# Kernel optimization log

Measured on AMD Instinct MI355X. Metric: run time of the kernel, lower is better.

## Reference

```python
import jax, jax.numpy as jnp
import numpy as np

B = 1 << 20
EMB = 8
N_BREEDS, N_TEMPS = 15, 9
HIDDENS = [128, 64, 32]
IN_DIM = (EMB * 2 + 9) * 2  # 50
EPS = 1e-5


def _encode_pet(breed, size, energy, temp, age, social, weight, breed_emb, temp_emb):
    # breed/temp: [B] int -> embedding gather [B,8]; size/energy -> one-hot [B,3]
    be = breed_emb[breed]
    te = temp_emb[temp]
    size_oh = jax.nn.one_hot(size, 3, dtype=be.dtype)
    energy_oh = jax.nn.one_hot(energy, 3, dtype=be.dtype)
    nums = jnp.stack([age / 15.0, social, weight / 100.0], axis=-1)  # [B,3]
    return jnp.concatenate([be, size_oh, energy_oh, te, nums], axis=-1)  # [B,25]


def _mlp(x, Ws, bs, gammas, betas, Wout, bout):
    for W, b, g, bt in zip(Ws, bs, gammas, betas):
        x = x @ W + b
        mu = jnp.mean(x, axis=0)
        var = jnp.mean(jnp.square(x - mu), axis=0)  # biased var (torch BN training)
        x = (x - mu) * jax.lax.rsqrt(var + EPS) * g + bt
        x = jax.nn.relu(x)
    x = x @ Wout + bout
    return jax.nn.sigmoid(x).squeeze(-1)  # [B]


def setup_inputs() -> dict:
    key = jax.random.key(0)
    ks = jax.random.split(key, 32)
    inp = {
        "pet1_breed": jax.random.randint(ks[0], (B,), 0, N_BREEDS, dtype=jnp.int32),
        "pet1_size": jax.random.randint(ks[1], (B,), 0, 3, dtype=jnp.int32),
        "pet1_energy": jax.random.randint(ks[2], (B,), 0, 3, dtype=jnp.int32),
        "pet1_temp": jax.random.randint(ks[3], (B,), 0, N_TEMPS, dtype=jnp.int32),
        "pet1_age": jax.random.uniform(ks[4], (B,)) * 15.0,
        "pet1_social": jax.random.uniform(ks[5], (B,)),
        "pet1_weight": jax.random.uniform(ks[6], (B,)) * 100.0,
        "pet2_breed": jax.random.randint(ks[7], (B,), 0, N_BREEDS, dtype=jnp.int32),
        "pet2_size": jax.random.randint(ks[8], (B,), 0, 3, dtype=jnp.int32),
        "pet2_energy": jax.random.randint(ks[9], (B,), 0, 3, dtype=jnp.int32),
        "pet2_temp": jax.random.randint(ks[10], (B,), 0, N_TEMPS, dtype=jnp.int32),
        "pet2_age": jax.random.uniform(ks[11], (B,)) * 15.0,
        "pet2_social": jax.random.uniform(ks[12], (B,)),
        "pet2_weight": jax.random.uniform(ks[13], (B,)) * 100.0,
        "breed_emb": jax.random.normal(ks[14], (N_BREEDS, EMB), dtype=jnp.float32),
        "temp_emb": jax.random.normal(ks[15], (N_TEMPS, EMB), dtype=jnp.float32),
    }
    prev = IN_DIM
    ki = 16
    for i, h in enumerate(HIDDENS, start=1):
        s = 1.0 / np.sqrt(prev)
        inp[f"W{i}"] = jax.random.uniform(ks[ki], (prev, h), minval=-s, maxval=s); ki += 1
        inp[f"b{i}"] = jax.random.uniform(ks[ki], (h,), minval=-s, maxval=s); ki += 1
        inp[f"gamma{i}"] = jnp.ones((h,), jnp.float32)
        inp[f"beta{i}"] = jnp.zeros((h,), jnp.float32)
        prev = h
    s = 1.0 / np.sqrt(prev)
    inp["W4"] = jax.random.uniform(ks[ki], (prev, 1), minval=-s, maxval=s); ki += 1
    inp["b4"] = jax.random.uniform(ks[ki], (1,), minval=-s, maxval=s)
    return inp


def reference(pet1_breed, pet1_size, pet1_energy, pet1_temp, pet1_age, pet1_social, pet1_weight,
              pet2_breed, pet2_size, pet2_energy, pet2_temp, pet2_age, pet2_social, pet2_weight,
              breed_emb, temp_emb,
              W1, b1, gamma1, beta1, W2, b2, gamma2, beta2, W3, b3, gamma3, beta3, W4, b4):
    f1 = _encode_pet(pet1_breed, pet1_size, pet1_energy, pet1_temp,
                     pet1_age, pet1_social, pet1_weight, breed_emb, temp_emb)
    f2 = _encode_pet(pet2_breed, pet2_size, pet2_energy, pet2_temp,
                     pet2_age, pet2_social, pet2_weight, breed_emb, temp_emb)
    x = jnp.concatenate([f1, f2], axis=-1)  # [B,50]
    return _mlp(x, [W1, W2, W3], [b1, b2, b3], [gamma1, gamma2, gamma3],
                [beta1, beta2, beta3], W4, b4)
```

## Files before the change

### kernel.cpp

```cpp
#include <hip/hip_runtime.h>
#include <hip/hip_bf16.h>

#define BATCH (1u<<20)
static constexpr float EPSBN = 1e-5f;
static constexpr float INV_B = 1.0f / (float)BATCH;

typedef unsigned int   uint;
typedef unsigned short ushort;

#define TSTR 132
#define NTABROWS 66
#define TBSTR 136
#define OFF_TBF    36864ULL
#define OFF_W2F    55296ULL
#define OFF_W3F    71680ULL
#define OFF_STATS  75776ULL
#define OFF_PARAMS 90112ULL
#define OFF_X2     98304ULL
#define T1_NEED    (98304ULL + 134217728ULL)

struct Ptrs {
  const int *br1,*sz1,*en1,*tp1; const float *ag1,*so1,*wt1;
  const int *br2,*sz2,*en2,*tp2; const float *ag2,*so2,*wt2;
  const float *bemb,*temb;
  const float *W1,*b1,*g1,*be1;
  const float *W2,*b2,*g2,*be2;
  const float *W3,*b3,*g3,*be3;
  const float *W4,*b4;
  float* ws; float* out;
};

typedef __attribute__((ext_vector_type(8))) short bf16x8;
typedef __attribute__((ext_vector_type(4))) float f32x4;

__device__ __forceinline__ float4 ld4(const float* p) {
  return *reinterpret_cast<const float4*>(p);
}
__device__ __forceinline__ void add4(float4& a, const float4 b) {
  a.x += b.x; a.y += b.y; a.z += b.z; a.w += b.w;
}
__device__ __forceinline__ void fma4s(float4& a, const float4 b, float s) {
  a.x = fmaf(b.x, s, a.x); a.y = fmaf(b.y, s, a.y);
  a.z = fmaf(b.z, s, a.z); a.w = fmaf(b.w, s, a.w);
}

__device__ __forceinline__ ushort bfb(float f) {
  union { __hip_bfloat16 h; ushort u; } cv; cv.h = __float2bfloat16(f); return cv.u;
}
__device__ __forceinline__ uint pk2(float a, float b) {
  return ((uint)bfb(b) << 16) | (uint)bfb(a);
}
__device__ __forceinline__ bf16x8 ldfrag(const void* p) {
  union { uint4 u; bf16x8 v; } cv; cv.u = *reinterpret_cast<const uint4*>(p); return cv.v;
}
__device__ __forceinline__ bf16x8 mkfrag(uint a, uint b, uint c, uint d) {
  union { uint4 u; bf16x8 v; } cv; cv.u = make_uint4(a,b,c,d); return cv.v;
}
__device__ __forceinline__ float bflo(uint w) { return __uint_as_float(w << 16); }
__device__ __forceinline__ float bfhi(uint w) { return __uint_as_float(w & 0xffff0000u); }

struct SIdx { int r[8]; float v[6]; };
__device__ __forceinline__ SIdx load_idx(const Ptrs& P, unsigned s) {
  SIdx o;
  o.r[0] = P.br1[s];      o.r[1] = 15 + P.tp1[s];
  o.r[2] = 24 + P.br2[s]; o.r[3] = 39 + P.tp2[s];
  o.r[4] = 48 + P.sz1[s]; o.r[5] = 51 + P.en1[s];
  o.r[6] = 54 + P.sz2[s]; o.r[7] = 57 + P.en2[s];
  o.v[0] = P.ag1[s]*(1.0f/15.0f); o.v[1] = P.so1[s]; o.v[2] = P.wt1[s]*0.01f;
  o.v[3] = P.ag2[s]*(1.0f/15.0f); o.v[4] = P.so2[s]; o.v[5] = P.wt2[s]*0.01f;
  return o;
}

__device__ __forceinline__ void load_rb(const Ptrs& P, unsigned s, int rb[8], float v[6]) {
  SIdx o = load_idx(P, s);
  #pragma unroll
  for (int i = 0; i < 8; ++i) rb[i] = o.r[i]*TSTR;
  #pragma unroll
  for (int i = 0; i < 6; ++i) v[i] = o.v[i];
}

__device__ __forceinline__ void stage_tab(const float* wsT, const float* params,
                                          float* Tl, bool bn1) {
  for (int i = threadIdx.x; i < NTABROWS*TSTR; i += blockDim.x) Tl[i] = wsT[i];
  if (bn1) {
    for (int i = threadIdx.x; i < 128; i += blockDim.x) {
      Tl[66*TSTR + i] = params[i];
      Tl[67*TSTR + i] = params[128 + i];
    }
  }
  __syncthreads();
}

__device__ __forceinline__ void x2_from_lds(const float* Tl, const int rb[8], const float v[6],
                                            const float* W2, const float* b2, float4 acc[16]) {
  #pragma unroll
  for (int j4 = 0; j4 < 16; ++j4) acc[j4] = ld4(b2 + j4*4);
  #pragma unroll 1
  for (int c4 = 0; c4 < 32; ++c4) {
    const int c = c4 * 4;
    float4 x = *reinterpret_cast<const float4*>(Tl + rb[0] + c);
    add4(x, *reinterpret_cast<const float4*>(Tl + rb[1] + c));
    add4(x, *reinterpret_cast<const float4*>(Tl + rb[2] + c));
    add4(x, *reinterpret_cast<const float4*>(Tl + rb[3] + c));
    add4(x, *reinterpret_cast<const float4*>(Tl + rb[4] + c));
    add4(x, *reinterpret_cast<const float4*>(Tl + rb[5] + c));
    add4(x, *reinterpret_cast<const float4*>(Tl + rb[6] + c));
    add4(x, *reinterpret_cast<const float4*>(Tl + rb[7] + c));
    #pragma unroll
    for (int m = 0; m < 6; ++m)
      fma4s(x, *reinterpret_cast<const float4*>(Tl + (60+m)*TSTR + c), v[m]);
    const float4 sc = *reinterpret_cast<const float4*>(Tl + 66*TSTR + c);
    const float4 sh = *reinterpret_cast<const float4*>(Tl + 67*TSTR + c);
    float hv[4];
    hv[0] = fmaxf(fmaf(x.x, sc.x, sh.x), 0.0f);
    hv[1] = fmaxf(fmaf(x.y, sc.y, sh.y), 0.0f);
    hv[2] = fmaxf(fmaf(x.z, sc.z, sh.z), 0.0f);
    hv[3] = fmaxf(fmaf(x.w, sc.w, sh.w), 0.0f);
    #pragma unroll
    for (int r = 0; r < 4; ++r) {
      const float hr = hv[r];
      const float4* w = reinterpret_cast<const float4*>(W2 + (c + r)*64);
      #pragma unroll
      for (int j4 = 0; j4 < 16; ++j4) fma4s(acc[j4], w[j4], hr);
    }
  }
}

__device__ __forceinline__ void x3_from_acc2(const float4 acc2[16], const Ptrs& P,
                                             const float* sc2, const float* sh2,
                                             float4 acc3[8]) {
  #pragma unroll
  for (int j4 = 0; j4 < 8; ++j4) acc3[j4] = ld4(P.b3 + j4*4);
  #pragma unroll
  for (int k4 = 0; k4 < 16; ++k4) {
    const float4 a = acc2[k4];
    const float4 sc = ld4(sc2 + k4*4), sh = ld4(sh2 + k4*4);
    const float hr[4] = {
      fmaxf(fmaf(a.x, sc.x, sh.x), 0.0f),
      fmaxf(fmaf(a.y, sc.y, sh.y), 0.0f),
      fmaxf(fmaf(a.z, sc.z, sh.z), 0.0f),
      fmaxf(fmaf(a.w, sc.w, sh.w), 0.0f)};
    #pragma unroll
    for (int r = 0; r < 4; ++r) {
      const float4* w = reinterpret_cast<const float4*>(P.W3 + (k4*4 + r)*32);
      #pragma unroll
      for (int j4 = 0; j4 < 8; ++j4) fma4s(acc3[j4], w[j4], hr[r]);
    }
  }
}

__device__ __forceinline__ float bfly_tail32(float st[32], int lane) {
#define BSTEP(D) { const bool h = (lane & D) != 0; \
  _Pragma("unroll") \
  for (int i = 0; i < D; ++i) { \
    float mine = h ? st[i] : st[i+D]; \
    float oth  = __shfl_xor(mine, D, 64); \
    float keep = h ? st[i+D] : st[i]; \
    st[i] = keep + oth; } }
  BSTEP(16) BSTEP(8) BSTEP(4) BSTEP(2) BSTEP(1)
#undef BSTEP
  return st[0];
}

template<bool SQ>
__device__ __forceinline__ float bfly64_from(const float4 acc[16], int lane) {
  float st[32];
  const bool hi = (lane & 32) != 0;
  #pragma unroll
  for (int j4 = 0; j4 < 8; ++j4) {
#define DO1(comp, idx) { \
    float lo = acc[j4].comp, hc = acc[j4+8].comp; \
    if (SQ) { lo *= lo; hc *= hc; } \
    float mine = hi ? lo : hc; \
    float keep = hi ? hc : lo; \
    st[4*j4+idx] = keep + __shfl_xor(mine, 32, 64); }
    DO1(x,0) DO1(y,1) DO1(z,2) DO1(w,3)
#undef DO1
  }
  return bfly_tail32(st, lane);
}

template<bool SQ>
__device__ __forceinline__ float bfly32_from(const float4 acc3[8], int lane) {
  float st[32];
  const bool hi = (lane & 32) != 0;
  #pragma unroll
  for (int j4 = 0; j4 < 8; ++j4) {
#define DO1(comp, idx) { \
    float vv = acc3[j4].comp; \
    if (SQ) vv *= vv; \
    float mine = hi ? vv : 0.0f; \
    float keep = hi ? 0.0f : vv; \
    st[4*j4+idx] = keep + __shfl_xor(mine, 32, 64); }
    DO1(x,0) DO1(y,1) DO1(z,2) DO1(w,3)
#undef DO1
  }
  return bfly_tail32(st, lane);
}


__global__ __launch_bounds__(256) void k_prep(Ptrs P) {
  const int t = threadIdx.x;
  float* T = P.ws;
  {
    float* st = (float*)((char*)P.ws + OFF_STATS);
    for (int i = t; i < 224*16; i += 256) st[i] = 0.0f;
  }
  if (t < 128) {
    const int c = t;
    for (int b = 0; b < 15; ++b) {
      float a1 = P.b1[c], a2 = 0.0f;
      #pragma unroll
      for (int e = 0; e < 8; ++e) {
        a1 = fmaf(P.bemb[b*8+e], P.W1[e*128 + c], a1);
        a2 = fmaf(P.bemb[b*8+e], P.W1[(25+e)*128 + c], a2);
      }
      T[b*TSTR + c] = a1; T[(24+b)*TSTR + c] = a2;
    }
    for (int tt = 0; tt < 9; ++tt) {
      float a1 = 0.0f, a2 = 0.0f;
      #pragma unroll
      for (int e = 0; e < 8; ++e) {
        a1 = fmaf(P.temb[tt*8+e], P.W1[(14+e)*128 + c], a1);
        a2 = fmaf(P.temb[tt*8+e], P.W1[(39+e)*128 + c], a2);
      }
      T[(15+tt)*TSTR + c] = a1; T[(39+tt)*TSTR + c] = a2;
    }
    #pragma unroll
    for (int i = 0; i < 3; ++i) {
      T[(48+i)*TSTR + c] = P.W1[(8+i)*128 + c];
      T[(51+i)*TSTR + c] = P.W1[(11+i)*128 + c];
      T[(54+i)*TSTR + c] = P.W1[(33+i)*128 + c];
      T[(57+i)*TSTR + c] = P.W1[(36+i)*128 + c];
    }
    const int cr[6] = {22,23,24,47,48,49};
    #pragma unroll
    for (int m = 0; m < 6; ++m) T[(60+m)*TSTR + c] = P.W1[cr[m]*128 + c];
  }
  __syncthreads();
  __hip_bfloat16* Tb = (__hip_bfloat16*)((char*)P.ws + OFF_TBF);
  for (int idx = t; idx < 66*128; idx += 256) {
    const int r = idx >> 7, c = idx & 127;
    Tb[r*TBSTR + c] = __float2bfloat16(T[r*TSTR + c]);
  }
  __hip_bfloat16* w2f = (__hip_bfloat16*)((char*)P.ws + OFF_W2F);
  for (int slot = t; slot < 1024; slot += 256) {
    const int fid = slot >> 6, l = slot & 63;
    const int mt = fid >> 2, kk = fid & 3, q = l >> 4, m = l & 15;
    #pragma unroll
    for (int e = 0; e < 8; ++e)
      w2f[slot*8 + e] = __float2bfloat16(P.W2[(kk*32 + 8*q + e)*64 + 16*mt + m]);
  }
  __hip_bfloat16* w3f = (__hip_bfloat16*)((char*)P.ws + OFF_W3F);
  for (int slot = t; slot < 256; slot += 256) {
    const int fid = slot >> 6, l = slot & 63;
    const int mt = fid >> 1, kk = fid & 1, q = l >> 4, m = l & 15;
    #pragma unroll
    for (int e = 0; e < 8; ++e)
      w3f[slot*8 + e] = __float2bfloat16(P.W3[(kk*32 + 8*q + e)*32 + 16*mt + m]);
  }
}

__global__ __launch_bounds__(512) void k_stats1(Ptrs P) {
  __shared__ __align__(16) __hip_bfloat16 Tb[60*TBSTR];
  __shared__ float sred[256];
  {
    const uint* src = (const uint*)((const char*)P.ws + OFF_TBF);
    uint* dst = (uint*)Tb;
    for (int i = threadIdx.x; i < 60*TBSTR/2; i += 512) dst[i] = src[i];
  }
  if (threadIdx.x < 256) sred[threadIdx.x] = 0.f;
  __syncthreads();
  const int lane = threadIdx.x & 63;
  const int q = lane >> 4, m16 = lane & 15;
  const __hip_bfloat16* Tbc = (const __hip_bfloat16*)((const char*)P.ws + OFF_TBF);
  const unsigned gw = (blockIdx.x*512 + threadIdx.x) >> 6;
  const unsigned nw = (gridDim.x*512) >> 6;
  const int kk = gw & 3;
  const unsigned t0 = gw >> 2, ts = nw >> 2;
  const int c = kk*32 + 8*q;
  float sums[8], sqs[8];
  #pragma unroll
  for (int i = 0; i < 8; ++i) { sums[i] = 0.f; sqs[i] = 0.f; }
  for (unsigned tt = t0; tt < (BATCH>>4); tt += ts) {
    const unsigned s = tt*16 + m16;
    const SIdx o = load_idx(P, s);
    float x[8];
    #pragma unroll
    for (int e = 0; e < 8; ++e) x[e] = 0.f;
    #pragma unroll
    for (int g = 0; g < 8; ++g) {
      const uint4 u = *reinterpret_cast<const uint4*>(Tb + o.r[g]*TBSTR + c);
      const uint w[4] = {u.x,u.y,u.z,u.w};
      #pragma unroll
      for (int j = 0; j < 4; ++j) { x[2*j] += bflo(w[j]); x[2*j+1] += bfhi(w[j]); }
    }
    #pragma unroll
    for (int m = 0; m < 6; ++m) {
      const uint4 u = *reinterpret_cast<const uint4*>(Tbc + (60+m)*TBSTR + c);
      const uint w[4] = {u.x,u.y,u.z,u.w};
      #pragma unroll
      for (int j = 0; j < 4; ++j) {
        x[2*j]   = fmaf(bflo(w[j]), o.v[m], x[2*j]);
        x[2*j+1] = fmaf(bfhi(w[j]), o.v[m], x[2*j+1]);
      }
    }
    #pragma unroll
    for (int e = 0; e < 8; ++e) {
      sums[e] += x[e];
      sqs[e]   = fmaf(x[e], x[e], sqs[e]);
    }
  }
  #pragma unroll
  for (int d = 1; d <= 8; d <<= 1) {
    #pragma unroll
    for (int i = 0; i < 8; ++i) {
      sums[i] += __shfl_xor(sums[i], d, 64);
      sqs[i]  += __shfl_xor(sqs[i],  d, 64);
    }
  }
  if (m16 == 0) {
    #pragma unroll
    for (int e = 0; e < 8; ++e) {
      atomicAdd(&sred[c + e], sums[e]);
      atomicAdd(&sred[128 + c + e], sqs[e]);
    }
  }
  __syncthreads();
  if (threadIdx.x < 128) {
    float* stat = (float*)((char*)P.ws + OFF_STATS) + (size_t)threadIdx.x*16;
    atomicAdd(stat,     sred[threadIdx.x]);
    atomicAdd(stat + 8, sred[128+threadIdx.x]);
  }
}

__global__ void k_finalize(Ptrs P, int nch, int entry0, int pofs,
                           const float* g, const float* be) {
  const int c = threadIdx.x;
  if (c >= nch) return;
  const float* stat = (const float*)((const char*)P.ws + OFF_STATS) + (size_t)(entry0 + c)*16;
  const float mean = stat[0] * INV_B;
  const float var  = stat[8] * INV_B - mean*mean;
  const float inv  = 1.0f / sqrtf(var + EPSBN);
  const float scale = g[c] * inv;
  float* params = (float*)((char*)P.ws + OFF_PARAMS);
  params[pofs + c]       = scale;
  params[pofs + nch + c] = be[c] - mean * scale;
}

__global__ __launch_bounds__(512) void k_l2m(Ptrs P) {
  __shared__ __align__(16) float Tl[60*TSTR];
  for (int i = threadIdx.x; i < 60*TSTR; i += 512) Tl[i] = P.ws[i];
  __syncthreads();
  const float* params = (const float*)((const char*)P.ws + OFF_PARAMS);
  const float* sc1 = params, *sh1 = params + 128;
  const float* contT = P.ws;
  const int lane = threadIdx.x & 63;
  const int q = lane >> 4, m16 = lane & 15;
  const char* w2fB = (const char*)P.ws + OFF_W2F;
  char* x2B = (char*)P.ws + OFF_X2;
  const unsigned nw = (gridDim.x*512) >> 6;
  const unsigned NT = BATCH >> 4;
  unsigned it = (blockIdx.x*512 + threadIdx.x) >> 6;
  if (it >= NT) return;
  SIdx cur = load_idx(P, it*16 + m16);
  while (true) {
    const unsigned itn = it + nw;
    const bool more = itn < NT;
    SIdx nxt;
    if (more) nxt = load_idx(P, itn*16 + m16);
    const unsigned s = it*16 + m16;
    int rb[8];
    #pragma unroll
    for (int i = 0; i < 8; ++i) rb[i] = cur.r[i]*TSTR;
    f32x4 D[4];
    #pragma unroll
    for (int mt = 0; mt < 4; ++mt) {
      const float4 b = ld4(P.b2 + 16*mt + 4*q);
      D[mt][0] = b.x; D[mt][1] = b.y; D[mt][2] = b.z; D[mt][3] = b.w;
    }
    #pragma unroll
    for (int kk = 0; kk < 4; ++kk) {
      const int c = kk*32 + 8*q;
      float4 xa = ld4(Tl + rb[0] + c);
      float4 xb = ld4(Tl + rb[0] + c + 4);
      #pragma unroll
      for (int g = 1; g < 8; ++g) {
        add4(xa, ld4(Tl + rb[g] + c));
        add4(xb, ld4(Tl + rb[g] + c + 4));
      }
      #pragma unroll
      for (int m = 0; m < 6; ++m) {
        fma4s(xa, ld4(contT + (60+m)*TSTR + c), cur.v[m]);
        fma4s(xb, ld4(contT + (60+m)*TSTR + c + 4), cur.v[m]);
      }
      const float4 sca = ld4(sc1 + c), sha = ld4(sh1 + c);
      const float4 scb = ld4(sc1 + c + 4), shb = ld4(sh1 + c + 4);
      const float h0 = fmaxf(fmaf(xa.x, sca.x, sha.x), 0.f);
      const float h1 = fmaxf(fmaf(xa.y, sca.y, sha.y), 0.f);
      const float h2 = fmaxf(fmaf(xa.z, sca.z, sha.z), 0.f);
      const float h3 = fmaxf(fmaf(xa.w, sca.w, sha.w), 0.f);
      const float h4 = fmaxf(fmaf(xb.x, scb.x, shb.x), 0.f);
      const float h5 = fmaxf(fmaf(xb.y, scb.y, shb.y), 0.f);
      const float h6 = fmaxf(fmaf(xb.z, scb.z, shb.z), 0.f);
      const float h7 = fmaxf(fmaf(xb.w, scb.w, shb.w), 0.f);
      const bf16x8 bf = mkfrag(pk2(h0,h1), pk2(h2,h3), pk2(h4,h5), pk2(h6,h7));
      #pragma unroll
      for (int mt = 0; mt < 4; ++mt) {
        const bf16x8 af = ldfrag(w2fB + (size_t)((mt*4+kk)*64 + lane)*16);
        D[mt] = __builtin_amdgcn_mfma_f32_16x16x32_bf16(af, bf, D[mt], 0, 0, 0);
      }
    }
    #pragma unroll
    for (int mt = 0; mt < 4; ++mt) {
      const uint lo = pk2(D[mt][0], D[mt][1]);
      const uint hi = pk2(D[mt][2], D[mt][3]);
      *reinterpret_cast<uint2*>(x2B + (size_t)s*128 + (16*mt + 4*q)*2) = make_uint2(lo, hi);
    }
    if (!more) break;
    cur = nxt; it = itn;
  }
}

__global__ __launch_bounds__(256) void k_stats2(Ptrs P) {
  const uint* x2u = (const uint*)((const char*)P.ws + OFF_X2);
  const int pid = threadIdx.x & 31;
  const int lane = threadIdx.x & 63;
  const int w = threadIdx.x >> 6;
  float slo = 0.f, shi = 0.f, qlo = 0.f, qhi = 0.f;
  const unsigned r0 = blockIdx.x*8 + (threadIdx.x >> 5);
  const unsigned rs = gridDim.x*8;
  #pragma unroll 4
  for (unsigned r = r0; r < BATCH; r += rs) {
    const uint u = x2u[(size_t)r*32 + pid];
    const float lo = bflo(u), hi = bfhi(u);
    slo += lo; shi += hi;
    qlo = fmaf(lo, lo, qlo); qhi = fmaf(hi, hi, qhi);
  }
  slo += __shfl_xor(slo, 32, 64); shi += __shfl_xor(shi, 32, 64);
  qlo += __shfl_xor(qlo, 32, 64); qhi += __shfl_xor(qhi, 32, 64);
  __shared__ float red[512];
  if (lane < 32) {
    red[w*64 + 2*pid]       = slo; red[w*64 + 2*pid + 1]       = shi;
    red[256 + w*64 + 2*pid] = qlo; red[256 + w*64 + 2*pid + 1] = qhi;
  }
  __syncthreads();
  if (threadIdx.x < 64) {
    const int c = threadIdx.x;
    const float s  = red[c] + red[64+c] + red[128+c] + red[192+c];
    const float qq = red[256+c] + red[320+c] + red[384+c] + red[448+c];
    float* stat = (float*)((char*)P.ws + OFF_STATS) + (size_t)(128 + c)*16;
    atomicAdd(stat, s); atomicAdd(stat + 8, qq);
  }
}

__global__ __launch_bounds__(256) void k_l3m(Ptrs P) {
  const float* params = (const float*)((const char*)P.ws + OFF_PARAMS);
  const float* sc2 = params + 256, *sh2 = params + 320;
  const int lane = threadIdx.x & 63;
  const int q = lane >> 4, m16 = lane & 15;
  const char* w3fB = (const char*)P.ws + OFF_W3F;
  char* xB = (char*)P.ws + OFF_X2;
  const unsigned nw = (gridDim.x*256) >> 6;
  const unsigned NT = BATCH >> 4;
  unsigned it = (blockIdx.x*256 + threadIdx.x) >> 6;
  if (it >= NT) return;
  unsigned s = it*16 + m16;
  uint4 u0 = *reinterpret_cast<const uint4*>(xB + (size_t)s*128 + q*16);
  uint4 u1 = *reinterpret_cast<const uint4*>(xB + (size_t)s*128 + 64 + q*16);
  while (true) {
    const unsigned itn = it + nw;
    const bool more = itn < NT;
    uint4 n0, n1;
    if (more) {
      const unsigned sn = itn*16 + m16;
      n0 = *reinterpret_cast<const uint4*>(xB + (size_t)sn*128 + q*16);
      n1 = *reinterpret_cast<const uint4*>(xB + (size_t)sn*128 + 64 + q*16);
    }
    f32x4 D[2];
    #pragma unroll
    for (int mt = 0; mt < 2; ++mt) {
      const float4 b = ld4(P.b3 + 16*mt + 4*q);
      D[mt][0] = b.x; D[mt][1] = b.y; D[mt][2] = b.z; D[mt][3] = b.w;
    }
    #pragma unroll
    for (int kk = 0; kk < 2; ++kk) {
      const uint4 u = (kk == 0) ? u0 : u1;
      const int c = kk*32 + 8*q;
      const float4 scA = ld4(sc2 + c), shA = ld4(sh2 + c);
      const float4 scB = ld4(sc2 + c + 4), shB = ld4(sh2 + c + 4);
      const uint w[4] = {u.x,u.y,u.z,u.w};
      const float h0 = fmaxf(fmaf(bflo(w[0]), scA.x, shA.x), 0.f);
      const float h1 = fmaxf(fmaf(bfhi(w[0]), scA.y, shA.y), 0.f);
      const float h2 = fmaxf(fmaf(bflo(w[1]), scA.z, shA.z), 0.f);
      const float h3 = fmaxf(fmaf(bfhi(w[1]), scA.w, shA.w), 0.f);
      const float h4 = fmaxf(fmaf(bflo(w[2]), scB.x, shB.x), 0.f);
      const float h5 = fmaxf(fmaf(bfhi(w[2]), scB.y, shB.y), 0.f);
      const float h6 = fmaxf(fmaf(bflo(w[3]), scB.z, shB.z), 0.f);
      const float h7 = fmaxf(fmaf(bfhi(w[3]), scB.w, shB.w), 0.f);
      const bf16x8 bf = mkfrag(pk2(h0,h1), pk2(h2,h3), pk2(h4,h5), pk2(h6,h7));
      #pragma unroll
      for (int mt = 0; mt < 2; ++mt) {
        const bf16x8 af = ldfrag(w3fB + (size_t)((mt*2+kk)*64 + lane)*16);
        D[mt] = __builtin_amdgcn_mfma_f32_16x16x32_bf16(af, bf, D[mt], 0, 0, 0);
      }
    }
    #pragma unroll
    for (int mt = 0; mt < 2; ++mt) {
      const uint lo = pk2(D[mt][0], D[mt][1]);
      const uint hi = pk2(D[mt][2], D[mt][3]);
      *reinterpret_cast<uint2*>(xB + (size_t)s*128 + (16*mt + 4*q)*2) = make_uint2(lo, hi);
    }
    if (!more) break;
    u0 = n0; u1 = n1; it = itn; s = it*16 + m16;
  }
}

__global__ __launch_bounds__(256) void k_stats3(Ptrs P) {
  const uint* xu = (const uint*)((const char*)P.ws + OFF_X2);
  const int pid = threadIdx.x & 15;
  const int lane = threadIdx.x & 63;
  const int w = threadIdx.x >> 6;
  float slo = 0.f, shi = 0.f, qlo = 0.f, qhi = 0.f;
  const unsigned r0 = blockIdx.x*16 + (threadIdx.x >> 4);
  const unsigned rs = gridDim.x*16;
  #pragma unroll 4
  for (unsigned r = r0; r < BATCH; r += rs) {
    const uint u = xu[(size_t)r*32 + pid];
    const float lo = bflo(u), hi = bfhi(u);
    slo += lo; shi += hi;
    qlo = fmaf(lo, lo, qlo); qhi = fmaf(hi, hi, qhi);
  }
  #pragma unroll
  for (int d = 16; d <= 32; d <<= 1) {
    slo += __shfl_xor(slo, d, 64); shi += __shfl_xor(shi, d, 64);
    qlo += __shfl_xor(qlo, d, 64); qhi += __shfl_xor(qhi, d, 64);
  }
  __shared__ float red[256];
  if (lane < 16) {
    red[w*32 + 2*pid]       = slo; red[w*32 + 2*pid + 1]       = shi;
    red[128 + w*32 + 2*pid] = qlo; red[128 + w*32 + 2*pid + 1] = qhi;
  }
  __syncthreads();
  if (threadIdx.x < 32) {
    const int c = threadIdx.x;
    const float s  = red[c] + red[32+c] + red[64+c] + red[96+c];
    const float qq = red[128+c] + red[160+c] + red[192+c] + red[224+c];
    float* stat = (float*)((char*)P.ws + OFF_STATS) + (size_t)(192 + c)*16;
    atomicAdd(stat, s); atomicAdd(stat + 8, qq);
  }
}

__global__ __launch_bounds__(256) void k_l4n(Ptrs P) {
  const float* params = (const float*)((const char*)P.ws + OFF_PARAMS);
  const float* sc3 = params + 384, *sh3 = params + 416;
  const char* xB = (const char*)P.ws + OFF_X2;
  const unsigned stride = gridDim.x * 256;
  for (unsigned s = blockIdx.x*256 + threadIdx.x; s < BATCH; s += stride) {
    float z = P.b4[0];
    #pragma unroll
    for (int c16 = 0; c16 < 4; ++c16) {
      const uint4 u = *reinterpret_cast<const uint4*>(xB + (size_t)s*128 + c16*16);
      const uint w[4] = {u.x,u.y,u.z,u.w};
      #pragma unroll
      for (int j = 0; j < 4; ++j) {
        const int ch = c16*8 + 2*j;
        const float hlo = fmaxf(fmaf(bflo(w[j]), sc3[ch],   sh3[ch]),   0.f);
        const float hhi = fmaxf(fmaf(bfhi(w[j]), sc3[ch+1], sh3[ch+1]), 0.f);
        z = fmaf(hlo, P.W4[ch], z);
        z = fmaf(hhi, P.W4[ch+1], z);
      }
    }
    P.out[s] = 1.0f / (1.0f + __expf(-z));
  }
}

__global__ __launch_bounds__(256) void k_l2r(Ptrs P) {
  __shared__ __align__(16) float Tl[68*TSTR];
  __shared__ float red[512];
  const float* params = (const float*)((const char*)P.ws + OFF_PARAMS);
  stage_tab(P.ws, params, Tl, true);
  const int lane = threadIdx.x & 63;
  float4 sums[16], sqs[16];
  #pragma unroll
  for (int j4 = 0; j4 < 16; ++j4) {
    sums[j4] = make_float4(0.f,0.f,0.f,0.f);
    sqs[j4]  = make_float4(0.f,0.f,0.f,0.f);
  }
  const unsigned stride = gridDim.x * 256;
  for (unsigned s = blockIdx.x*256 + threadIdx.x; s < BATCH; s += stride) {
    int rb[8]; float v[6];
    load_rb(P, s, rb, v);
    float4 acc[16];
    x2_from_lds(Tl, rb, v, P.W2, P.b2, acc);
    #pragma unroll
    for (int j4 = 0; j4 < 16; ++j4) {
      add4(sums[j4], acc[j4]);
      sqs[j4].x = fmaf(acc[j4].x, acc[j4].x, sqs[j4].x);
      sqs[j4].y = fmaf(acc[j4].y, acc[j4].y, sqs[j4].y);
      sqs[j4].z = fmaf(acc[j4].z, acc[j4].z, sqs[j4].z);
      sqs[j4].w = fmaf(acc[j4].w, acc[j4].w, sqs[j4].w);
    }
  }
  const float psum = bfly64_from<false>(sums, lane);
  const float psq  = bfly64_from<false>(sqs,  lane);
  red[threadIdx.x] = psum; red[256 + threadIdx.x] = psq;
  __syncthreads();
  const int t = threadIdx.x;
  if (t < 64) {
    const float s0 = red[t] + red[t+64] + red[t+128] + red[t+192];
    const float q0 = red[256+t] + red[256+t+64] + red[256+t+128] + red[256+t+192];
    float* stat = (float*)((char*)P.ws + OFF_STATS) + (size_t)(128 + t)*16;
    atomicAdd(stat, s0); atomicAdd(stat + 8, q0);
  }
}

__global__ __launch_bounds__(256) void k_l3_rec(Ptrs P) {
  __shared__ __align__(16) float Tl[68*TSTR];
  __shared__ float red[512];
  const float* params = (const float*)((const char*)P.ws + OFF_PARAMS);
  stage_tab(P.ws, params, Tl, true);
  const float* sc2 = params + 256, *sh2 = params + 320;
  const int lane = threadIdx.x & 63;
  float4 sums3[8], sqs3[8];
  #pragma unroll
  for (int j4 = 0; j4 < 8; ++j4) {
    sums3[j4] = make_float4(0.f,0.f,0.f,0.f);
    sqs3[j4]  = make_float4(0.f,0.f,0.f,0.f);
  }
  const unsigned stride = gridDim.x * 256;
  for (unsigned s = blockIdx.x*256 + threadIdx.x; s < BATCH; s += stride) {
    int rb[8]; float v[6];
    load_rb(P, s, rb, v);
    float4 acc2[16];
    x2_from_lds(Tl, rb, v, P.W2, P.b2, acc2);
    float4 acc3[8];
    x3_from_acc2(acc2, P, sc2, sh2, acc3);
    #pragma unroll
    for (int j4 = 0; j4 < 8; ++j4) {
      add4(sums3[j4], acc3[j4]);
      sqs3[j4].x = fmaf(acc3[j4].x, acc3[j4].x, sqs3[j4].x);
      sqs3[j4].y = fmaf(acc3[j4].y, acc3[j4].y, sqs3[j4].y);
      sqs3[j4].z = fmaf(acc3[j4].z, acc3[j4].z, sqs3[j4].z);
      sqs3[j4].w = fmaf(acc3[j4].w, acc3[j4].w, sqs3[j4].w);
    }
  }
  const float psum = bfly32_from<false>(sums3, lane);
  const float psq  = bfly32_from<false>(sqs3,  lane);
  red[threadIdx.x] = psum; red[256 + threadIdx.x] = psq;
  __syncthreads();
  const int t = threadIdx.x;
  if (t < 32) {
    const float s0 = red[t] + red[t+64] + red[t+128] + red[t+192];
    const float q0 = red[256+t] + red[256+t+64] + red[256+t+128] + red[256+t+192];
    float* stat = (float*)((char*)P.ws + OFF_STATS) + (size_t)(192 + t)*16;
    atomicAdd(stat, s0); atomicAdd(stat + 8, q0);
  }
}

__global__ __launch_bounds__(256) void k_l4_rec(Ptrs P) {
  __shared__ __align__(16) float Tl[68*TSTR];
  const float* params = (const float*)((const char*)P.ws + OFF_PARAMS);
  stage_tab(P.ws, params, Tl, true);
  const float* sc2 = params + 256, *sh2 = params + 320;
  const float* sc3 = params + 384, *sh3 = params + 416;
  const unsigned stride = gridDim.x * 256;
  for (unsigned s = blockIdx.x*256 + threadIdx.x; s < BATCH; s += stride) {
    int rb[8]; float v[6];
    load_rb(P, s, rb, v);
    float4 acc2[16];
    x2_from_lds(Tl, rb, v, P.W2, P.b2, acc2);
    float4 acc3[8];
    x3_from_acc2(acc2, P, sc2, sh2, acc3);
    float z = P.b4[0];
    #pragma unroll
    for (int k4 = 0; k4 < 8; ++k4) {
      const float4 a = acc3[k4];
      const float4 sc = ld4(sc3 + k4*4), sh = ld4(sh3 + k4*4);
      z = fmaf(fmaxf(fmaf(a.x, sc.x, sh.x), 0.0f), P.W4[k4*4+0], z);
      z = fmaf(fmaxf(fmaf(a.y, sc.y, sh.y), 0.0f), P.W4[k4*4+1], z);
      z = fmaf(fmaxf(fmaf(a.z, sc.z, sh.z), 0.0f), P.W4[k4*4+2], z);
      z = fmaf(fmaxf(fmaf(a.w, sc.w, sh.w), 0.0f), P.W4[k4*4+3], z);
    }
    P.out[s] = 1.0f / (1.0f + __expf(-z));
  }
}


extern "C" void kernel_launch(void* const* d_in, const int* in_sizes, int n_in,
                              void* d_out, int out_size, void* d_ws, size_t ws_size,
                              hipStream_t stream) {
  Ptrs P;
  P.br1 = (const int*)d_in[0];  P.sz1 = (const int*)d_in[1];
  P.en1 = (const int*)d_in[2];  P.tp1 = (const int*)d_in[3];
  P.ag1 = (const float*)d_in[4]; P.so1 = (const float*)d_in[5]; P.wt1 = (const float*)d_in[6];
  P.br2 = (const int*)d_in[7];  P.sz2 = (const int*)d_in[8];
  P.en2 = (const int*)d_in[9];  P.tp2 = (const int*)d_in[10];
  P.ag2 = (const float*)d_in[11]; P.so2 = (const float*)d_in[12]; P.wt2 = (const float*)d_in[13];
  P.bemb = (const float*)d_in[14]; P.temb = (const float*)d_in[15];
  P.W1 = (const float*)d_in[16]; P.b1 = (const float*)d_in[17];
  P.g1 = (const float*)d_in[18]; P.be1 = (const float*)d_in[19];
  P.W2 = (const float*)d_in[20]; P.b2 = (const float*)d_in[21];
  P.g2 = (const float*)d_in[22]; P.be2 = (const float*)d_in[23];
  P.W3 = (const float*)d_in[24]; P.b3 = (const float*)d_in[25];
  P.g3 = (const float*)d_in[26]; P.be3 = (const float*)d_in[27];
  P.W4 = (const float*)d_in[28]; P.b4 = (const float*)d_in[29];
  P.ws = (float*)d_ws; P.out = (float*)d_out;

  const bool t1 = ws_size >= T1_NEED;

  hipLaunchKernelGGL(k_prep, dim3(1), dim3(256), 0, stream, P);
  hipLaunchKernelGGL(k_stats1, dim3(1024), dim3(512), 0, stream, P);
  hipLaunchKernelGGL(k_finalize, dim3(1), dim3(128), 0, stream, P, 128, 0, 0, P.g1, P.be1);
  if (t1) {
    hipLaunchKernelGGL(k_l2m, dim3(1024), dim3(512), 0, stream, P);
    hipLaunchKernelGGL(k_stats2, dim3(1024), dim3(256), 0, stream, P);
    hipLaunchKernelGGL(k_finalize, dim3(1), dim3(64), 0, stream, P, 64, 128, 256, P.g2, P.be2);
    hipLaunchKernelGGL(k_l3m, dim3(2048), dim3(256), 0, stream, P);
    hipLaunchKernelGGL(k_stats3, dim3(1024), dim3(256), 0, stream, P);
    hipLaunchKernelGGL(k_finalize, dim3(1), dim3(32), 0, stream, P, 32, 192, 384, P.g3, P.be3);
    hipLaunchKernelGGL(k_l4n, dim3(2048), dim3(256), 0, stream, P);
  } else {
    hipLaunchKernelGGL(k_l2r, dim3(1024), dim3(256), 0, stream, P);
    hipLaunchKernelGGL(k_finalize, dim3(1), dim3(64), 0, stream, P, 64, 128, 256, P.g2, P.be2);
    hipLaunchKernelGGL(k_l3_rec, dim3(1024), dim3(256), 0, stream, P);
    hipLaunchKernelGGL(k_finalize, dim3(1), dim3(32), 0, stream, P, 32, 192, 384, P.g3, P.be3);
    hipLaunchKernelGGL(k_l4_rec, dim3(2048), dim3(256), 0, stream, P);
  }
}
```

Measured before the change: 611.8 us.

## Fuse BN statistics into layer kernels and fold finalize into consumers

Layer-2 and layer-3 BN statistics are now accumulated inside the matmul kernels via shuffle and atomic reductions, which removes the separate stats2/stats3 passes that re-read the large activation buffers. The finalize kernels are folded into the consuming kernels, which compute scale and shift in shared memory. Layer-3 output goes to a dense 64-byte-stride buffer when workspace allows, so the last layer reads less data. Stats1 uses the fp32 table instead of a bf16 copy, with software-prefetched indices. The trade-off is more registers and atomics per kernel, plus a small per-block recomputation of the BN parameters.

```diff
diff --git a/kernel.cpp b/kernel.cpp
--- a/kernel.cpp
+++ b/kernel.cpp
@@ -10,14 +10,14 @@
 
 #define TSTR 132
 #define NTABROWS 66
-#define TBSTR 136
-#define OFF_TBF    36864ULL
 #define OFF_W2F    55296ULL
 #define OFF_W3F    71680ULL
 #define OFF_STATS  75776ULL
 #define OFF_PARAMS 90112ULL
 #define OFF_X2     98304ULL
+#define OFF_X3D    (98304ULL + 134217728ULL)
 #define T1_NEED    (98304ULL + 134217728ULL)
+#define T2_NEED    (98304ULL + 134217728ULL + 67108864ULL)
 
 struct Ptrs {
   const int *br1,*sz1,*en1,*tp1; const float *ag1,*so1,*wt1;
@@ -36,6 +36,12 @@
 __device__ __forceinline__ float4 ld4(const float* p) {
   return *reinterpret_cast<const float4*>(p);
 }
+__device__ __forceinline__ float4 f4add(float4 a, float4 b) {
+  return make_float4(a.x+b.x, a.y+b.y, a.z+b.z, a.w+b.w);
+}
+__device__ __forceinline__ float4 f4fma(float4 a, float4 w, float s) {
+  return make_float4(fmaf(w.x,s,a.x), fmaf(w.y,s,a.y), fmaf(w.z,s,a.z), fmaf(w.w,s,a.w));
+}
 __device__ __forceinline__ void add4(float4& a, const float4 b) {
   a.x += b.x; a.y += b.y; a.z += b.z; a.w += b.w;
 }
@@ -71,6 +77,21 @@
   return o;
 }
 
+__device__ __forceinline__ float4 gather4(const float* Tl, const float* contT,
+                                          const int rb[8], const float v[6], int c) {
+  float4 A = f4add(f4add(ld4(Tl+rb[0]+c), ld4(Tl+rb[1]+c)),
+                   f4add(ld4(Tl+rb[2]+c), ld4(Tl+rb[3]+c)));
+  float4 B = f4add(f4add(ld4(Tl+rb[4]+c), ld4(Tl+rb[5]+c)),
+                   f4add(ld4(Tl+rb[6]+c), ld4(Tl+rb[7]+c)));
+  A = f4fma(A, ld4(contT + 60*TSTR + c), v[0]);
+  A = f4fma(A, ld4(contT + 61*TSTR + c), v[1]);
+  A = f4fma(A, ld4(contT + 62*TSTR + c), v[2]);
+  B = f4fma(B, ld4(contT + 63*TSTR + c), v[3]);
+  B = f4fma(B, ld4(contT + 64*TSTR + c), v[4]);
+  B = f4fma(B, ld4(contT + 65*TSTR + c), v[5]);
+  return f4add(A, B);
+}
+
 __device__ __forceinline__ void load_rb(const Ptrs& P, unsigned s, int rb[8], float v[6]) {
   SIdx o = load_idx(P, s);
   #pragma unroll
@@ -98,17 +119,7 @@
   #pragma unroll 1
   for (int c4 = 0; c4 < 32; ++c4) {
     const int c = c4 * 4;
-    float4 x = *reinterpret_cast<const float4*>(Tl + rb[0] + c);
-    add4(x, *reinterpret_cast<const float4*>(Tl + rb[1] + c));
-    add4(x, *reinterpret_cast<const float4*>(Tl + rb[2] + c));
-    add4(x, *reinterpret_cast<const float4*>(Tl + rb[3] + c));
-    add4(x, *reinterpret_cast<const float4*>(Tl + rb[4] + c));
-    add4(x, *reinterpret_cast<const float4*>(Tl + rb[5] + c));
-    add4(x, *reinterpret_cast<const float4*>(Tl + rb[6] + c));
-    add4(x, *reinterpret_cast<const float4*>(Tl + rb[7] + c));
-    #pragma unroll
-    for (int m = 0; m < 6; ++m)
-      fma4s(x, *reinterpret_cast<const float4*>(Tl + (60+m)*TSTR + c), v[m]);
+    float4 x = gather4(Tl, Tl, rb, v, c);
     const float4 sc = *reinterpret_cast<const float4*>(Tl + 66*TSTR + c);
     const float4 sh = *reinterpret_cast<const float4*>(Tl + 67*TSTR + c);
     float hv[4];
@@ -238,11 +249,6 @@
     for (int m = 0; m < 6; ++m) T[(60+m)*TSTR + c] = P.W1[cr[m]*128 + c];
   }
   __syncthreads();
-  __hip_bfloat16* Tb = (__hip_bfloat16*)((char*)P.ws + OFF_TBF);
-  for (int idx = t; idx < 66*128; idx += 256) {
-    const int r = idx >> 7, c = idx & 127;
-    Tb[r*TBSTR + c] = __float2bfloat16(T[r*TSTR + c]);
-  }
   __hip_bfloat16* w2f = (__hip_bfloat16*)((char*)P.ws + OFF_W2F);
   for (int slot = t; slot < 1024; slot += 256) {
     const int fid = slot >> 6, l = slot & 63;
@@ -262,69 +268,63 @@
 }
 
 __global__ __launch_bounds__(512) void k_stats1(Ptrs P) {
-  __shared__ __align__(16) __hip_bfloat16 Tb[60*TBSTR];
+  __shared__ __align__(16) float Tl[60*TSTR];
   __shared__ float sred[256];
-  {
-    const uint* src = (const uint*)((const char*)P.ws + OFF_TBF);
-    uint* dst = (uint*)Tb;
-    for (int i = threadIdx.x; i < 60*TBSTR/2; i += 512) dst[i] = src[i];
-  }
+  for (int i = threadIdx.x; i < 60*TSTR; i += 512) Tl[i] = P.ws[i];
   if (threadIdx.x < 256) sred[threadIdx.x] = 0.f;
   __syncthreads();
   const int lane = threadIdx.x & 63;
   const int q = lane >> 4, m16 = lane & 15;
-  const __hip_bfloat16* Tbc = (const __hip_bfloat16*)((const char*)P.ws + OFF_TBF);
+  const float* contT = P.ws;
   const unsigned gw = (blockIdx.x*512 + threadIdx.x) >> 6;
   const unsigned nw = (gridDim.x*512) >> 6;
   const int kk = gw & 3;
-  const unsigned t0 = gw >> 2, ts = nw >> 2;
   const int c = kk*32 + 8*q;
-  float sums[8], sqs[8];
-  #pragma unroll
-  for (int i = 0; i < 8; ++i) { sums[i] = 0.f; sqs[i] = 0.f; }
-  for (unsigned tt = t0; tt < (BATCH>>4); tt += ts) {
-    const unsigned s = tt*16 + m16;
-    const SIdx o = load_idx(P, s);
-    float x[8];
-    #pragma unroll
-    for (int e = 0; e < 8; ++e) x[e] = 0.f;
-    #pragma unroll
-    for (int g = 0; g < 8; ++g) {
-      const uint4 u = *reinterpret_cast<const uint4*>(Tb + o.r[g]*TBSTR + c);
-      const uint w[4] = {u.x,u.y,u.z,u.w};
-      #pragma unroll
-      for (int j = 0; j < 4; ++j) { x[2*j] += bflo(w[j]); x[2*j+1] += bfhi(w[j]); }
-    }
-    #pragma unroll
-    for (int m = 0; m < 6; ++m) {
-      const uint4 u = *reinterpret_cast<const uint4*>(Tbc + (60+m)*TBSTR + c);
-      const uint w[4] = {u.x,u.y,u.z,u.w};
-      #pragma unroll
-      for (int j = 0; j < 4; ++j) {
-        x[2*j]   = fmaf(bflo(w[j]), o.v[m], x[2*j]);
-        x[2*j+1] = fmaf(bfhi(w[j]), o.v[m], x[2*j+1]);
-      }
-    }
-    #pragma unroll
-    for (int e = 0; e < 8; ++e) {
-      sums[e] += x[e];
-      sqs[e]   = fmaf(x[e], x[e], sqs[e]);
-    }
+  const unsigned NT = BATCH >> 4;
+  unsigned it = gw >> 2;
+  const unsigned ts = nw >> 2;
+  float4 sa = make_float4(0,0,0,0), sb = sa, qa = sa, qb = sa;
+  bool active = it < NT;
+  SIdx cur;
+  if (active) cur = load_idx(P, it*16 + m16);
+  while (active) {
+    const unsigned itn = it + ts;
+    const bool more = itn < NT;
+    SIdx nxt;
+    if (more) nxt = load_idx(P, itn*16 + m16);
+    int rb[8];
+    #pragma unroll
+    for (int i = 0; i < 8; ++i) rb[i] = cur.r[i]*TSTR;
+    const float4 xa = gather4(Tl, contT, rb, cur.v, c);
+    const float4 xb = gather4(Tl, contT, rb, cur.v, c + 4);
+    add4(sa, xa); add4(sb, xb);
+    qa.x = fmaf(xa.x, xa.x, qa.x); qa.y = fmaf(xa.y, xa.y, qa.y);
+    qa.z = fmaf(xa.z, xa.z, qa.z); qa.w = fmaf(xa.w, xa.w, qa.w);
+    qb.x = fmaf(xb.x, xb.x, qb.x); qb.y = fmaf(xb.y, xb.y, qb.y);
+    qb.z = fmaf(xb.z, xb.z, qb.z); qb.w = fmaf(xb.w, xb.w, qb.w);
+    if (!more) break;
+    cur = nxt; it = itn;
   }
   #pragma unroll
   for (int d = 1; d <= 8; d <<= 1) {
-    #pragma unroll
-    for (int i = 0; i < 8; ++i) {
-      sums[i] += __shfl_xor(sums[i], d, 64);
-      sqs[i]  += __shfl_xor(sqs[i],  d, 64);
-    }
+    sa.x += __shfl_xor(sa.x, d, 64); sa.y += __shfl_xor(sa.y, d, 64);
+    sa.z += __shfl_xor(sa.z, d, 64); sa.w += __shfl_xor(sa.w, d, 64);
+    sb.x += __shfl_xor(sb.x, d, 64); sb.y += __shfl_xor(sb.y, d, 64);
+    sb.z += __shfl_xor(sb.z, d, 64); sb.w += __shfl_xor(sb.w, d, 64);
+    qa.x += __shfl_xor(qa.x, d, 64); qa.y += __shfl_xor(qa.y, d, 64);
+    qa.z += __shfl_xor(qa.z, d, 64); qa.w += __shfl_xor(qa.w, d, 64);
+    qb.x += __shfl_xor(qb.x, d, 64); qb.y += __shfl_xor(qb.y, d, 64);
+    qb.z += __shfl_xor(qb.z, d, 64); qb.w += __shfl_xor(qb.w, d, 64);
   }
   if (m16 == 0) {
-    #pragma unroll
-    for (int e = 0; e < 8; ++e) {
-      atomicAdd(&sred[c + e], sums[e]);
-      atomicAdd(&sred[128 + c + e], sqs[e]);
-    }
+    atomicAdd(&sred[c+0], sa.x); atomicAdd(&sred[c+1], sa.y);
+    atomicAdd(&sred[c+2], sa.z); atomicAdd(&sred[c+3], sa.w);
+    atomicAdd(&sred[c+4], sb.x); atomicAdd(&sred[c+5], sb.y);
+    atomicAdd(&sred[c+6], sb.z); atomicAdd(&sred[c+7], sb.w);
+    atomicAdd(&sred[128+c+0], qa.x); atomicAdd(&sred[128+c+1], qa.y);
+    atomicAdd(&sred[128+c+2], qa.z); atomicAdd(&sred[128+c+3], qa.w);
+    atomicAdd(&sred[128+c+4], qb.x); atomicAdd(&sred[128+c+5], qb.y);
+    atomicAdd(&sred[128+c+6], qb.z); atomicAdd(&sred[128+c+7], qb.w);
   }
   __syncthreads();
   if (threadIdx.x < 128) {
@@ -350,10 +350,19 @@
 
 __global__ __launch_bounds__(512) void k_l2m(Ptrs P) {
   __shared__ __align__(16) float Tl[60*TSTR];
+  __shared__ __align__(16) float bn[256];
+  __shared__ float sred[128];
   for (int i = threadIdx.x; i < 60*TSTR; i += 512) Tl[i] = P.ws[i];
-  __syncthreads();
-  const float* params = (const float*)((const char*)P.ws + OFF_PARAMS);
-  const float* sc1 = params, *sh1 = params + 128;
+  if (threadIdx.x < 128) {
+    const float* stat = (const float*)((const char*)P.ws + OFF_STATS) + (size_t)threadIdx.x*16;
+    const float mean = stat[0] * INV_B;
+    const float var  = stat[8] * INV_B - mean*mean;
+    const float scale = P.g1[threadIdx.x] / sqrtf(var + EPSBN);
+    bn[threadIdx.x]       = scale;
+    bn[128 + threadIdx.x] = P.be1[threadIdx.x] - mean * scale;
+    sred[threadIdx.x] = 0.f;
+  }
+  __syncthreads();
   const float* contT = P.ws;
   const int lane = threadIdx.x & 63;
   const int q = lane >> 4, m16 = lane & 15;
@@ -362,9 +371,13 @@
   const unsigned nw = (gridDim.x*512) >> 6;
   const unsigned NT = BATCH >> 4;
   unsigned it = (blockIdx.x*512 + threadIdx.x) >> 6;
-  if (it >= NT) return;
-  SIdx cur = load_idx(P, it*16 + m16);
-  while (true) {
+  f32x4 ssum[4], ssq[4];
+  #pragma unroll
+  for (int mt = 0; mt < 4; ++mt) { ssum[mt] = (f32x4){0,0,0,0}; ssq[mt] = (f32x4){0,0,0,0}; }
+  bool active = it < NT;
+  SIdx cur;
+  if (active) cur = load_idx(P, it*16 + m16);
+  while (active) {
     const unsigned itn = it + nw;
     const bool more = itn < NT;
     SIdx nxt;
@@ -382,20 +395,10 @@
     #pragma unroll
     for (int kk = 0; kk < 4; ++kk) {
       const int c = kk*32 + 8*q;
-      float4 xa = ld4(Tl + rb[0] + c);
-      float4 xb = ld4(Tl + rb[0] + c + 4);
-      #pragma unroll
-      for (int g = 1; g < 8; ++g) {
-        add4(xa, ld4(Tl + rb[g] + c));
-        add4(xb, ld4(Tl + rb[g] + c + 4));
-      }
-      #pragma unroll
-      for (int m = 0; m < 6; ++m) {
-        fma4s(xa, ld4(contT + (60+m)*TSTR + c), cur.v[m]);
-        fma4s(xb, ld4(contT + (60+m)*TSTR + c + 4), cur.v[m]);
-      }
-      const float4 sca = ld4(sc1 + c), sha = ld4(sh1 + c);
-      const float4 scb = ld4(sc1 + c + 4), shb = ld4(sh1 + c + 4);
+      const float4 xa = gather4(Tl, contT, rb, cur.v, c);
+      const float4 xb = gather4(Tl, contT, rb, cur.v, c + 4);
+      const float4 sca = ld4(bn + c), sha = ld4(bn + 128 + c);
+      const float4 scb = ld4(bn + c + 4), shb = ld4(bn + 128 + c + 4);
       const float h0 = fmaxf(fmaf(xa.x, sca.x, sha.x), 0.f);
       const float h1 = fmaxf(fmaf(xa.y, sca.y, sha.y), 0.f);
       const float h2 = fmaxf(fmaf(xa.z, sca.z, sha.z), 0.f);
@@ -413,6 +416,12 @@
     }
     #pragma unroll
     for (int mt = 0; mt < 4; ++mt) {
+      #pragma unroll
+      for (int r = 0; r < 4; ++r) {
+        const float d = D[mt][r];
+        ssum[mt][r] += d;
+        ssq[mt][r]   = fmaf(d, d, ssq[mt][r]);
+      }
       const uint lo = pk2(D[mt][0], D[mt][1]);
       const uint hi = pk2(D[mt][2], D[mt][3]);
       *reinterpret_cast<uint2*>(x2B + (size_t)s*128 + (16*mt + 4*q)*2) = make_uint2(lo, hi);
@@ -420,55 +429,69 @@
     if (!more) break;
     cur = nxt; it = itn;
   }
-}
-
-__global__ __launch_bounds__(256) void k_stats2(Ptrs P) {
-  const uint* x2u = (const uint*)((const char*)P.ws + OFF_X2);
-  const int pid = threadIdx.x & 31;
-  const int lane = threadIdx.x & 63;
-  const int w = threadIdx.x >> 6;
-  float slo = 0.f, shi = 0.f, qlo = 0.f, qhi = 0.f;
-  const unsigned r0 = blockIdx.x*8 + (threadIdx.x >> 5);
-  const unsigned rs = gridDim.x*8;
-  #pragma unroll 4
-  for (unsigned r = r0; r < BATCH; r += rs) {
-    const uint u = x2u[(size_t)r*32 + pid];
-    const float lo = bflo(u), hi = bfhi(u);
-    slo += lo; shi += hi;
-    qlo = fmaf(lo, lo, qlo); qhi = fmaf(hi, hi, qhi);
-  }
-  slo += __shfl_xor(slo, 32, 64); shi += __shfl_xor(shi, 32, 64);
-  qlo += __shfl_xor(qlo, 32, 64); qhi += __shfl_xor(qhi, 32, 64);
-  __shared__ float red[512];
-  if (lane < 32) {
-    red[w*64 + 2*pid]       = slo; red[w*64 + 2*pid + 1]       = shi;
-    red[256 + w*64 + 2*pid] = qlo; red[256 + w*64 + 2*pid + 1] = qhi;
+  #pragma unroll
+  for (int d = 1; d <= 8; d <<= 1) {
+    #pragma unroll
+    for (int mt = 0; mt < 4; ++mt) {
+      #pragma unroll
+      for (int r = 0; r < 4; ++r) {
+        ssum[mt][r] += __shfl_xor(ssum[mt][r], d, 64);
+        ssq[mt][r]  += __shfl_xor(ssq[mt][r],  d, 64);
+      }
+    }
+  }
+  if (m16 == 0) {
+    #pragma unroll
+    for (int mt = 0; mt < 4; ++mt) {
+      #pragma unroll
+      for (int r = 0; r < 4; ++r) {
+        const int ch = 16*mt + 4*q + r;
+        atomicAdd(&sred[ch], ssum[mt][r]);
+        atomicAdd(&sred[64+ch], ssq[mt][r]);
+      }
+    }
   }
   __syncthreads();
   if (threadIdx.x < 64) {
-    const int c = threadIdx.x;
-    const float s  = red[c] + red[64+c] + red[128+c] + red[192+c];
-    const float qq = red[256+c] + red[320+c] + red[384+c] + red[448+c];
-    float* stat = (float*)((char*)P.ws + OFF_STATS) + (size_t)(128 + c)*16;
-    atomicAdd(stat, s); atomicAdd(stat + 8, qq);
-  }
-}
-
-__global__ __launch_bounds__(256) void k_l3m(Ptrs P) {
-  const float* params = (const float*)((const char*)P.ws + OFF_PARAMS);
-  const float* sc2 = params + 256, *sh2 = params + 320;
+    float* stat = (float*)((char*)P.ws + OFF_STATS) + (size_t)(128 + threadIdx.x)*16;
+    atomicAdd(stat, sred[threadIdx.x]);
+    atomicAdd(stat + 8, sred[64+threadIdx.x]);
+  }
+}
+
+__global__ __launch_bounds__(256) void k_l3m(Ptrs P, int dense) {
+  __shared__ __align__(16) float bn[128];
+  __shared__ float sred[64];
+  if (threadIdx.x < 64) {
+    const float* stat = (const float*)((const char*)P.ws + OFF_STATS) + (size_t)(128 + threadIdx.x)*16;
+    const float mean = stat[0] * INV_B;
+    const float var  = stat[8] * INV_B - mean*mean;
+    const float scale = P.g2[threadIdx.x] / sqrtf(var + EPSBN);
+    bn[threadIdx.x]      = scale;
+    bn[64 + threadIdx.x] = P.be2[threadIdx.x] - mean * scale;
+    sred[threadIdx.x] = 0.f;
+  }
+  __syncthreads();
   const int lane = threadIdx.x & 63;
   const int q = lane >> 4, m16 = lane & 15;
   const char* w3fB = (const char*)P.ws + OFF_W3F;
-  char* xB = (char*)P.ws + OFF_X2;
+  const char* xB = (const char*)P.ws + OFF_X2;
+  char* x3B = dense ? ((char*)P.ws + OFF_X3D) : ((char*)P.ws + OFF_X2);
+  const size_t x3str = dense ? 64 : 128;
   const unsigned nw = (gridDim.x*256) >> 6;
   const unsigned NT = BATCH >> 4;
   unsigned it = (blockIdx.x*256 + threadIdx.x) >> 6;
-  if (it >= NT) return;
+  f32x4 ssum[2], ssq[2];
+  #pragma unroll
+  for (int mt = 0; mt < 2; ++mt) { ssum[mt] = (f32x4){0,0,0,0}; ssq[mt] = (f32x4){0,0,0,0}; }
+  bool active = it < NT;
   unsigned s = it*16 + m16;
-  uint4 u0 = *reinterpret_cast<const uint4*>(xB + (size_t)s*128 + q*16);
-  uint4 u1 = *reinterpret_cast<const uint4*>(xB + (size_t)s*128 + 64 + q*16);
-  while (true) {
+  uint4 u0, u1;
+  if (active) {
+    u0 = *reinterpret_cast<const uint4*>(xB + (size_t)s*128 + q*16);
+    u1 = *reinterpret_cast<const uint4*>(xB + (size_t)s*128 + 64 + q*16);
+  }
+  while (active) {
     const unsigned itn = it + nw;
     const bool more = itn < NT;
     uint4 n0, n1;
@@ -487,8 +510,8 @@
     for (int kk = 0; kk < 2; ++kk) {
       const uint4 u = (kk == 0) ? u0 : u1;
       const int c = kk*32 + 8*q;
-      const float4 scA = ld4(sc2 + c), shA = ld4(sh2 + c);
-      const float4 scB = ld4(sc2 + c + 4), shB = ld4(sh2 + c + 4);
+      const float4 scA = ld4(bn + c), shA = ld4(bn + 64 + c);
+      const float4 scB = ld4(bn + c + 4), shB = ld4(bn + 64 + c + 4);
       const uint w[4] = {u.x,u.y,u.z,u.w};
       const float h0 = fmaxf(fmaf(bflo(w[0]), scA.x, shA.x), 0.f);
       const float h1 = fmaxf(fmaf(bfhi(w[0]), scA.y, shA.y), 0.f);
@@ -507,60 +530,69 @@
     }
     #pragma unroll
     for (int mt = 0; mt < 2; ++mt) {
+      #pragma unroll
+      for (int r = 0; r < 4; ++r) {
+        const float d = D[mt][r];
+        ssum[mt][r] += d;
+        ssq[mt][r]   = fmaf(d, d, ssq[mt][r]);
+      }
       const uint lo = pk2(D[mt][0], D[mt][1]);
       const uint hi = pk2(D[mt][2], D[mt][3]);
-      *reinterpret_cast<uint2*>(xB + (size_t)s*128 + (16*mt + 4*q)*2) = make_uint2(lo, hi);
+      *reinterpret_cast<uint2*>(x3B + (size_t)s*x3str + (16*mt + 4*q)*2) = make_uint2(lo, hi);
     }
     if (!more) break;
     u0 = n0; u1 = n1; it = itn; s = it*16 + m16;
   }
-}
-
-__global__ __launch_bounds__(256) void k_stats3(Ptrs P) {
-  const uint* xu = (const uint*)((const char*)P.ws + OFF_X2);
-  const int pid = threadIdx.x & 15;
-  const int lane = threadIdx.x & 63;
-  const int w = threadIdx.x >> 6;
-  float slo = 0.f, shi = 0.f, qlo = 0.f, qhi = 0.f;
-  const unsigned r0 = blockIdx.x*16 + (threadIdx.x >> 4);
-  const unsigned rs = gridDim.x*16;
-  #pragma unroll 4
-  for (unsigned r = r0; r < BATCH; r += rs) {
-    const uint u = xu[(size_t)r*32 + pid];
-    const float lo = bflo(u), hi = bfhi(u);
-    slo += lo; shi += hi;
-    qlo = fmaf(lo, lo, qlo); qhi = fmaf(hi, hi, qhi);
-  }
-  #pragma unroll
-  for (int d = 16; d <= 32; d <<= 1) {
-    slo += __shfl_xor(slo, d, 64); shi += __shfl_xor(shi, d, 64);
-    qlo += __shfl_xor(qlo, d, 64); qhi += __shfl_xor(qhi, d, 64);
-  }
-  __shared__ float red[256];
-  if (lane < 16) {
-    red[w*32 + 2*pid]       = slo; red[w*32 + 2*pid + 1]       = shi;
-    red[128 + w*32 + 2*pid] = qlo; red[128 + w*32 + 2*pid + 1] = qhi;
+  #pragma unroll
+  for (int d = 1; d <= 8; d <<= 1) {
+    #pragma unroll
+    for (int mt = 0; mt < 2; ++mt) {
+      #pragma unroll
+      for (int r = 0; r < 4; ++r) {
+        ssum[mt][r] += __shfl_xor(ssum[mt][r], d, 64);
+        ssq[mt][r]  += __shfl_xor(ssq[mt][r],  d, 64);
+      }
+    }
+  }
+  if (m16 == 0) {
+    #pragma unroll
+    for (int mt = 0; mt < 2; ++mt) {
+      #pragma unroll
+      for (int r = 0; r < 4; ++r) {
+        const int ch = 16*mt + 4*q + r;
+        atomicAdd(&sred[ch], ssum[mt][r]);
+        atomicAdd(&sred[32+ch], ssq[mt][r]);
+      }
+    }
   }
   __syncthreads();
   if (threadIdx.x < 32) {
-    const int c = threadIdx.x;
-    const float s  = red[c] + red[32+c] + red[64+c] + red[96+c];
-    const float qq = red[128+c] + red[160+c] + red[192+c] + red[224+c];
-    float* stat = (float*)((char*)P.ws + OFF_STATS) + (size_t)(192 + c)*16;
-    atomicAdd(stat, s); atomicAdd(stat + 8, qq);
-  }
-}
-
-__global__ __launch_bounds__(256) void k_l4n(Ptrs P) {
-  const float* params = (const float*)((const char*)P.ws + OFF_PARAMS);
-  const float* sc3 = params + 384, *sh3 = params + 416;
-  const char* xB = (const char*)P.ws + OFF_X2;
+    float* stat = (float*)((char*)P.ws + OFF_STATS) + (size_t)(192 + threadIdx.x)*16;
+    atomicAdd(stat, sred[threadIdx.x]);
+    atomicAdd(stat + 8, sred[32+threadIdx.x]);
+  }
+}
+
+__global__ __launch_bounds__(256) void k_l4n(Ptrs P, int dense) {
+  __shared__ float bn[64];
+  if (threadIdx.x < 32) {
+    const float* stat = (const float*)((const char*)P.ws + OFF_STATS) + (size_t)(192 + threadIdx.x)*16;
+    const float mean = stat[0] * INV_B;
+    const float var  = stat[8] * INV_B - mean*mean;
+    const float scale = P.g3[threadIdx.x] / sqrtf(var + EPSBN);
+    bn[threadIdx.x]      = scale;
+    bn[32 + threadIdx.x] = P.be3[threadIdx.x] - mean * scale;
+  }
+  __syncthreads();
+  const float* sc3 = bn, *sh3 = bn + 32;
+  const char* xB = dense ? ((const char*)P.ws + OFF_X3D) : ((const char*)P.ws + OFF_X2);
+  const size_t xstr = dense ? 64 : 128;
   const unsigned stride = gridDim.x * 256;
   for (unsigned s = blockIdx.x*256 + threadIdx.x; s < BATCH; s += stride) {
     float z = P.b4[0];
     #pragma unroll
     for (int c16 = 0; c16 < 4; ++c16) {
-      const uint4 u = *reinterpret_cast<const uint4*>(xB + (size_t)s*128 + c16*16);
+      const uint4 u = *reinterpret_cast<const uint4*>(xB + (size_t)s*xstr + c16*16);
       const uint w[4] = {u.x,u.y,u.z,u.w};
       #pragma unroll
       for (int j = 0; j < 4; ++j) {
@@ -708,19 +740,16 @@
   P.ws = (float*)d_ws; P.out = (float*)d_out;
 
   const bool t1 = ws_size >= T1_NEED;
+  const int dense = (ws_size >= T2_NEED) ? 1 : 0;
 
   hipLaunchKernelGGL(k_prep, dim3(1), dim3(256), 0, stream, P);
   hipLaunchKernelGGL(k_stats1, dim3(1024), dim3(512), 0, stream, P);
-  hipLaunchKernelGGL(k_finalize, dim3(1), dim3(128), 0, stream, P, 128, 0, 0, P.g1, P.be1);
   if (t1) {
     hipLaunchKernelGGL(k_l2m, dim3(1024), dim3(512), 0, stream, P);
-    hipLaunchKernelGGL(k_stats2, dim3(1024), dim3(256), 0, stream, P);
-    hipLaunchKernelGGL(k_finalize, dim3(1), dim3(64), 0, stream, P, 64, 128, 256, P.g2, P.be2);
-    hipLaunchKernelGGL(k_l3m, dim3(2048), dim3(256), 0, stream, P);
-    hipLaunchKernelGGL(k_stats3, dim3(1024), dim3(256), 0, stream, P);
-    hipLaunchKernelGGL(k_finalize, dim3(1), dim3(32), 0, stream, P, 32, 192, 384, P.g3, P.be3);
-    hipLaunchKernelGGL(k_l4n, dim3(2048), dim3(256), 0, stream, P);
+    hipLaunchKernelGGL(k_l3m, dim3(2048), dim3(256), 0, stream, P, dense);
+    hipLaunchKernelGGL(k_l4n, dim3(2048), dim3(256), 0, stream, P, dense);
   } else {
+    hipLaunchKernelGGL(k_finalize, dim3(1), dim3(128), 0, stream, P, 128, 0, 0, P.g1, P.be1);
     hipLaunchKernelGGL(k_l2r, dim3(1024), dim3(256), 0, stream, P);
     hipLaunchKernelGGL(k_finalize, dim3(1), dim3(64), 0, stream, P, 64, 128, 256, P.g2, P.be2);
     hipLaunchKernelGGL(k_l3_rec, dim3(1024), dim3(256), 0, stream, P);
```

After: 693.6 us. +13.4%, slower.
